# Kernel optimization log

Hardware: AMD Instinct MI355X
Metric: run time of the kernel (lower is better)

## Reference

```python
import jax, jax.numpy as jnp
import numpy as np

H = 1024          # hidden_size
K = 128           # MAX_LINK_CANDIDATES (cap applies to both keys and values)
EPS = 1e-8


def _spatial_features(kb, vb):
    """kb: [B,K,4] key boxes, vb: [B,V,4] value boxes -> [B,K,V,8].
    Vectorized version of _compute_spatial_features_pair over all (key,value) pairs."""
    kcx = (kb[..., 0] + kb[..., 2]) / 2
    kcy = (kb[..., 1] + kb[..., 3]) / 2
    vcx = (vb[..., 0] + vb[..., 2]) / 2
    vcy = (vb[..., 1] + vb[..., 3]) / 2
    dx = vcx[:, None, :] - kcx[:, :, None]                      # [B,K,V]
    dy = vcy[:, None, :] - kcy[:, :, None]
    dist = jnp.sqrt(dx ** 2 + dy ** 2 + EPS)
    angle = jnp.arctan2(dy, dx)
    kh = kb[..., 3] - kb[..., 1]
    vh = vb[..., 3] - vb[..., 1]
    h_ov = jnp.clip(jnp.minimum(kb[..., 3][:, :, None], vb[..., 3][:, None, :])
                    - jnp.maximum(kb[..., 1][:, :, None], vb[..., 1][:, None, :]), 0)
    h_align = h_ov / (jnp.minimum(kh[:, :, None], vh[:, None, :]) + EPS)
    kw = kb[..., 2] - kb[..., 0]
    vw = vb[..., 2] - vb[..., 0]
    v_ov = jnp.clip(jnp.minimum(kb[..., 2][:, :, None], vb[..., 2][:, None, :])
                    - jnp.maximum(kb[..., 0][:, :, None], vb[..., 0][:, None, :]), 0)
    v_align = v_ov / (jnp.minimum(kw[:, :, None], vw[:, None, :]) + EPS)
    area_ratio = (vh * vw)[:, None, :] / ((kh * kw)[:, :, None] + EPS)
    aspect = (vw / (vh + EPS))[:, None, :] / ((kw / (kh + EPS))[:, :, None])
    return jnp.stack([dx, dy, dist, angle, h_align, v_align, area_ratio, aspect], axis=-1)


def setup_inputs() -> dict:
    key = jax.random.key(0)
    ks = jax.random.split(key, 20)
    B, S = 4, 2048
    sequence_output = jax.random.normal(ks[0], (B, S, H), dtype=jnp.float32)
    entity_logits = jax.random.normal(ks[1], (B, S, 3), dtype=jnp.float32)
    base = jax.random.uniform(ks[2], (B, S, 2), dtype=jnp.float32) * 0.9
    size = jax.random.uniform(ks[3], (B, S, 2), dtype=jnp.float32) * 0.09 + 0.01
    bboxes = jnp.concatenate([base, base + size], axis=-1)      # valid x1<x2, y1<y2
    attention_mask = jnp.ones((B, S), dtype=jnp.int32)
    s = 1.0 / np.sqrt(H)
    inp = {
        "sequence_output": sequence_output,
        "entity_logits": entity_logits,
        "bboxes": bboxes,
        "attention_mask": attention_mask,
        "Wk": jax.random.normal(ks[4], (H, H), jnp.float32) * s,
        "bk": jnp.zeros((H,), jnp.float32),
        "Wv": jax.random.normal(ks[5], (H, H), jnp.float32) * s,
        "bv": jnp.zeros((H,), jnp.float32),
        "Wbil": jax.random.normal(ks[6], (H, H), jnp.float32) * s,   # bilinear weight (out=1 squeezed)
        "bbil": jnp.zeros((), jnp.float32),
        "Ws1": jax.random.normal(ks[7], (8, 64), jnp.float32) * (1.0 / np.sqrt(8)),
        "bs1": jnp.zeros((64,), jnp.float32),
        "Ws2": jax.random.normal(ks[8], (64, 32), jnp.float32) * (1.0 / np.sqrt(64)),
        "bs2": jnp.zeros((32,), jnp.float32),
        "Wf1": jax.random.normal(ks[9], (33, 16), jnp.float32) * (1.0 / np.sqrt(33)),
        "bf1": jnp.zeros((16,), jnp.float32),
        "Wf2": jax.random.normal(ks[10], (16, 1), jnp.float32) * 0.25,
        "bf2": jnp.zeros((1,), jnp.float32),
    }
    return inp


def reference(sequence_output, entity_logits, bboxes, attention_mask,
              Wk, bk, Wv, bv, Wbil, bbil, Ws1, bs1, Ws2, bs2, Wf1, bf1, Wf2, bf2):
    # Candidate selection: top-K tokens by class confidence among predicted keys/values.
    probs = jax.nn.softmax(entity_logits, axis=-1)
    preds = jnp.argmax(entity_logits, axis=-1)                  # [B,S]
    valid = attention_mask == 1
    key_conf = jnp.where((preds == 1) & valid, probs[..., 1], -jnp.inf)
    val_conf = jnp.where((preds == 2) & valid, probs[..., 2], -jnp.inf)
    _, key_idx = jax.lax.top_k(key_conf, K)                     # [B,K]
    _, val_idx = jax.lax.top_k(val_conf, K)

    seq_k = jnp.take_along_axis(sequence_output, key_idx[..., None], axis=1)  # [B,K,H]
    seq_v = jnp.take_along_axis(sequence_output, val_idx[..., None], axis=1)
    key_reps = seq_k @ Wk + bk                                  # dropout is identity at eval
    val_reps = seq_v @ Wv + bv

    # Bilinear scoring: k^T W v  -> [B,K,V] (chunking in torch is a memory detail, same math)
    biaffine = jnp.einsum('bkh,hg,bvg->bkv', key_reps, Wbil, val_reps) + bbil

    key_boxes = jnp.take_along_axis(bboxes, key_idx[..., None], axis=1)       # [B,K,4]
    val_boxes = jnp.take_along_axis(bboxes, val_idx[..., None], axis=1)
    sf = _spatial_features(key_boxes, val_boxes)                              # [B,K,V,8]
    spatial = jax.nn.relu(sf @ Ws1 + bs1) @ Ws2 + bs2                         # [B,K,V,32]

    combined = jnp.concatenate([biaffine[..., None], spatial], axis=-1)       # [B,K,V,33]
    scores = (jax.nn.relu(combined @ Wf1 + bf1) @ Wf2 + bf2)[..., 0]          # [B,K,V]
    return scores, key_idx, val_idx
```

## Files before the change

kernel.cpp:

```cpp
#include <hip/hip_runtime.h>
#include <hip/hip_bf16.h>
#include <math.h>

#define B_ 4
#define S_ 2048
#define H_ 1024
#define KC 128
#define EPSF 1e-8f

typedef __attribute__((ext_vector_type(8))) short bf16x8;
typedef __attribute__((ext_vector_type(4))) float f32x4;

#define B2F_LO(u) __uint_as_float((u) << 16)
#define B2F_HI(u) __uint_as_float((u) & 0xffff0000u)

static __device__ inline unsigned short f2b(float f) {
    unsigned u = __float_as_uint(f);
    return (unsigned short)((u + 0x7fffu + ((u >> 16) & 1u)) >> 16);
}

static __device__ inline void gload16(const void* g, void* l) {
    __builtin_amdgcn_global_load_lds(
        (const __attribute__((address_space(1))) unsigned int*)g,
        (__attribute__((address_space(3))) unsigned int*)l, 16, 0, 0);
}

static __device__ inline unsigned long long shflx64(unsigned long long v, int m) {
    int lo = __shfl_xor((int)(unsigned)(v & 0xffffffffull), m, 64);
    int hi = __shfl_xor((int)(unsigned)(v >> 32), m, 64);
    return ((unsigned long long)(unsigned)hi << 32) | (unsigned)lo;
}

#define CROSS_STAGE(k, j) do {                                              \
    const int lm = (j) >> 3;                                                \
    const bool upL  = (((lane) * 8) & (k)) == 0;                            \
    const bool lowr = ((lane) & lm) == 0;                                   \
    _Pragma("unroll")                                                       \
    for (int r = 0; r < 8; ++r) {                                           \
        unsigned long long o = shflx64(e[r], lm);                           \
        e[r] = ((upL == lowr) == (e[r] < o)) ? e[r] : o;                    \
    }                                                                       \
} while (0)

#define INTRA_STAGE(j, k) do {                                              \
    _Pragma("unroll")                                                       \
    for (int r = 0; r < 8; ++r) if (!(r & (j))) {                           \
        bool up = ((((lane) * 8 + r) & (k)) == 0);                          \
        unsigned long long a = e[r], b = e[r | (j)];                        \
        if (up ? (a > b) : (a < b)) { e[r] = b; e[r | (j)] = a; }           \
    }                                                                       \
} while (0)

static __device__ inline void wave_sort512(unsigned long long e[8], int lane) {
    INTRA_STAGE(1, 2);
    INTRA_STAGE(2, 4);  INTRA_STAGE(1, 4);
    INTRA_STAGE(4, 8);  INTRA_STAGE(2, 8);  INTRA_STAGE(1, 8);
    CROSS_STAGE(16, 8);
    INTRA_STAGE(4, 16); INTRA_STAGE(2, 16); INTRA_STAGE(1, 16);
    CROSS_STAGE(32, 16); CROSS_STAGE(32, 8);
    INTRA_STAGE(4, 32); INTRA_STAGE(2, 32); INTRA_STAGE(1, 32);
    CROSS_STAGE(64, 32); CROSS_STAGE(64, 16); CROSS_STAGE(64, 8);
    INTRA_STAGE(4, 64); INTRA_STAGE(2, 64); INTRA_STAGE(1, 64);
    CROSS_STAGE(128, 64); CROSS_STAGE(128, 32); CROSS_STAGE(128, 16);
    CROSS_STAGE(128, 8);
    INTRA_STAGE(4, 128); INTRA_STAGE(2, 128); INTRA_STAGE(1, 128);
    CROSS_STAGE(256, 128); CROSS_STAGE(256, 64); CROSS_STAGE(256, 32);
    CROSS_STAGE(256, 16); CROSS_STAGE(256, 8);
    INTRA_STAGE(4, 256); INTRA_STAGE(2, 256); INTRA_STAGE(1, 256);
    CROSS_STAGE(512, 256); CROSS_STAGE(512, 128); CROSS_STAGE(512, 64);
    CROSS_STAGE(512, 32); CROSS_STAGE(512, 16); CROSS_STAGE(512, 8);
    INTRA_STAGE(4, 512); INTRA_STAGE(2, 512); INTRA_STAGE(1, 512);
}

static __device__ inline void topk_block(
    const float* logits, const int* mask, int blk,
    int* key_idx, int* val_idx, float* out_idx_base,
    unsigned long long* cand, int tid)
{
    const int b   = blk >> 1;
    const int cls = (blk & 1) ? 2 : 1;
    const int wv = tid >> 6, lane = tid & 63;
    unsigned long long e[8];
    #pragma unroll
    for (int r = 0; r < 8; ++r) {
        int s = wv * 512 + lane * 8 + r;
        float l0 = logits[(b * S_ + s) * 3 + 0];
        float l1 = logits[(b * S_ + s) * 3 + 1];
        float l2 = logits[(b * S_ + s) * 3 + 2];
        int pred = 0; float bl = l0;
        if (l1 > bl) { bl = l1; pred = 1; }
        if (l2 > bl) { bl = l2; pred = 2; }
        float c = -1.0f;
        if (pred == cls && mask[b * S_ + s] == 1) {
            double m = (double)bl;
            double e0 = exp((double)l0 - m);
            double e1 = exp((double)l1 - m);
            double e2 = exp((double)l2 - m);
            c = (float)(((cls == 1) ? e1 : e2) / (e0 + e1 + e2));
        }
        unsigned int u = __float_as_uint(c);
        unsigned int mono = (u & 0x80000000u) ? ~u : (u | 0x80000000u);
        e[r] = ((unsigned long long)(~mono) << 32) | (unsigned int)s;
    }
    wave_sort512(e, lane);
    if (lane < 16) {
        #pragma unroll
        for (int r = 0; r < 8; ++r) cand[wv * 128 + lane * 8 + r] = e[r];
    }
    __syncthreads();
    if (wv == 0) {
        #pragma unroll
        for (int r = 0; r < 8; ++r) e[r] = cand[lane * 8 + r];
        wave_sort512(e, lane);
        if (lane < 16) {
            int* idx_out = (blk & 1) ? (val_idx + b * KC) : (key_idx + b * KC);
            float* oidx  = out_idx_base + ((blk & 1) ? B_ * KC : 0) + b * KC;
            #pragma unroll
            for (int r = 0; r < 8; ++r) {
                int sel = (int)(e[r] & 0xffffffffu);
                idx_out[lane * 8 + r] = sel;
                oidx[lane * 8 + r] = (float)sel;
            }
        }
    }
}

__global__ __launch_bounds__(256) void prep_kernel(
    const float* __restrict__ Wk, const float* __restrict__ Wv,
    const float* __restrict__ Wbil, unsigned short* __restrict__ Wt,
    const float* __restrict__ logits, const int* __restrict__ mask,
    int* __restrict__ key_idx, int* __restrict__ val_idx,
    const float* __restrict__ Ws1, const float* __restrict__ Ws2,
    const float* __restrict__ Wf1,
    unsigned short* __restrict__ Ws1T_b, unsigned short* __restrict__ Ws2_b,
    unsigned short* __restrict__ Wf1T_b, float* __restrict__ Wf1c0,
    float* __restrict__ out_idx)
{
    __shared__ float tile[32][33];
    __shared__ unsigned long long cand[512];
    const int tid = threadIdx.x;
    if (blockIdx.x < 3072) {
        const int z = blockIdx.x >> 10;
        const int remb = blockIdx.x & 1023;
        const float* Win = (z == 0) ? Wk : (z == 1) ? Wv : Wbil;
        unsigned short* out = Wt + (size_t)z * H_ * H_;
        const int n0 = (remb & 31) * 32, k0 = (remb >> 5) * 32;
        const int r = tid >> 3, c0 = (tid & 7) * 4;
        float4 v = *(const float4*)(Win + (size_t)(k0 + r) * H_ + n0 + c0);
        tile[r][c0 + 0] = v.x; tile[r][c0 + 1] = v.y;
        tile[r][c0 + 2] = v.z; tile[r][c0 + 3] = v.w;
        __syncthreads();
        short4 o;
        o.x = (short)f2b(tile[c0 + 0][r]);
        o.y = (short)f2b(tile[c0 + 1][r]);
        o.z = (short)f2b(tile[c0 + 2][r]);
        o.w = (short)f2b(tile[c0 + 3][r]);
        *(short4*)(out + (size_t)(n0 + r) * H_ + k0 + c0) = o;
        return;
    }
    if (blockIdx.x == 3080) {
        for (int i = tid; i < 512; i += 256) {
            int j = i >> 3, ii = i & 7;
            Ws1T_b[i] = f2b(Ws1[ii * 64 + j]);
        }
        for (int i = tid; i < 2048; i += 256) Ws2_b[i] = f2b(Ws2[i]);
        for (int i = tid; i < 512; i += 256) {
            int t = i >> 5, q = i & 31;
            Wf1T_b[i] = f2b(Wf1[(1 + q) * 16 + t]);
        }
        if (tid < 16) Wf1c0[tid] = Wf1[tid];
        return;
    }
    topk_block(logits, mask, blockIdx.x - 3072, key_idx, val_idx, out_idx,
               cand, tid);
}

__global__ __launch_bounds__(256) void gatherconv_kernel(
    const float* __restrict__ seq,
    const int* __restrict__ key_idx, const int* __restrict__ val_idx,
    unsigned short* __restrict__ Abf)
{
    const int row = blockIdx.x;
    const int tid = threadIdx.x;
    int b, srow;
    if (row < 512) { b = row >> 7; srow = key_idx[row]; }
    else           { b = (row - 512) >> 7; srow = val_idx[row - 512]; }
    const float* src = seq + ((size_t)b * S_ + srow) * H_ + tid * 4;
    float4 v = *(const float4*)src;
    short4 o;
    o.x = (short)f2b(v.x); o.y = (short)f2b(v.y);
    o.z = (short)f2b(v.z); o.w = (short)f2b(v.w);
    *(short4*)(Abf + (size_t)row * H_ + tid * 4) = o;
}

__global__ __launch_bounds__(256) void gemm_lds_kernel(
    const unsigned short* __restrict__ Ab,
    const unsigned short* __restrict__ Wt,
    const float* __restrict__ b0, const float* __restrict__ b1,
    unsigned short* __restrict__ Cout)
{
    __shared__ __align__(16) char As[64 * 512];
    __shared__ __align__(16) char Bs[64 * 512];

    const int NW8 = gridDim.x >> 3;
    int sw = ((int)blockIdx.x & 7) * NW8 + ((int)blockIdx.x >> 3);
    const int z  = sw >> 7;
    const int r2 = sw & 127;
    const int n0 = (r2 >> 3) * 64;
    const int m0 = (r2 & 7) * 64;

    Ab   += (size_t)z * 512 * H_;
    Cout += (size_t)z * 512 * H_;
    const unsigned short* Wz = Wt + (size_t)z * H_ * H_;
    const float* bias = z ? b1 : b0;

    const int tid  = threadIdx.x;
    const int lane = tid & 63, wv = tid >> 6;
    const int r = lane & 15, g = lane >> 4;
    const int mh = (wv >> 1) * 32, nh = (wv & 1) * 32;

    f32x4 acc[2][2] = {};

    for (int k0 = 0; k0 < H_; k0 += 256) {
        #pragma unroll
        for (int q = 0; q < 8; ++q) {
            const int seg = wv * 8 + q;
            const int row = (seg << 1) | (lane >> 5);
            const int gch = (lane & 31) ^ (row & 7);
            gload16(Ab + (size_t)(m0 + row) * H_ + k0 + gch * 8,
                    As + seg * 1024);
            gload16(Wz + (size_t)(n0 + row) * H_ + k0 + gch * 8,
                    Bs + seg * 1024);
        }
        __syncthreads();
        #pragma unroll
        for (int kk = 0; kk < 8; ++kk) {
            const int c = kk * 4 + g;
            bf16x8 av[2], bv[2];
            #pragma unroll
            for (int i = 0; i < 2; ++i) {
                const int row = mh + i * 16 + r;
                av[i] = *(const bf16x8*)(As + row * 512 + ((c ^ (row & 7)) << 4));
            }
            #pragma unroll
            for (int j = 0; j < 2; ++j) {
                const int row = nh + j * 16 + r;
                bv[j] = *(const bf16x8*)(Bs + row * 512 + ((c ^ (row & 7)) << 4));
            }
            #pragma unroll
            for (int i = 0; i < 2; ++i)
                #pragma unroll
                for (int j = 0; j < 2; ++j)
                    acc[i][j] = __builtin_amdgcn_mfma_f32_16x16x32_bf16(
                        av[i], bv[j], acc[i][j], 0, 0, 0);
        }
        __syncthreads();
    }

    const int orow = (lane >> 4) * 4, ocol = lane & 15;
    #pragma unroll
    for (int i = 0; i < 2; ++i)
        #pragma unroll
        for (int j = 0; j < 2; ++j) {
            const int n = n0 + nh + j * 16 + ocol;
            const float bv_ = bias ? bias[n] : 0.0f;
            #pragma unroll
            for (int gg = 0; gg < 4; ++gg)
                Cout[(size_t)(m0 + mh + i * 16 + orow + gg) * H_ + n]
                    = f2b(acc[i][j][gg] + bv_);
        }
}

__global__ __launch_bounds__(512) void biasp_kernel(
    const unsigned short* __restrict__ kbt,
    const unsigned short* __restrict__ vrep,
    const float* __restrict__ bbil, const float* __restrict__ bboxes,
    const int* __restrict__ key_idx, const int* __restrict__ val_idx,
    const unsigned short* __restrict__ Ws1T_b,
    const float* __restrict__ bs1,
    const unsigned short* __restrict__ Ws2_b,
    const float* __restrict__ bs2,
    const unsigned short* __restrict__ Wf1T_b,
    const float* __restrict__ Wf1c0,
    const float* __restrict__ bf1,
    const float* __restrict__ Wf2, const float* __restrict__ bf2,
    float* __restrict__ out)
{
    __shared__ float part[8][16][16];
    __shared__ uint4 sW1[64];
    __shared__ uint4 sW2[256];
    __shared__ uint4 sWf[64];
    __shared__ float sbs1[64];
    __shared__ float sbs2[32];
    __shared__ float sWf1c0[16];
    __shared__ float sbf1[16];
    __shared__ float sWf2[16];

    const int tid = threadIdx.x;
    if (tid < 64)  sW1[tid] = ((const uint4*)Ws1T_b)[tid];
    if (tid < 256) sW2[tid] = ((const uint4*)Ws2_b)[tid];
    if (tid >= 256 && tid < 320) sWf[tid - 256] = ((const uint4*)Wf1T_b)[tid - 256];
    if (tid >= 320 && tid < 384) sbs1[tid - 320] = bs1[tid - 320];
    if (tid >= 384 && tid < 416) sbs2[tid - 384] = bs2[tid - 384];
    if (tid >= 416 && tid < 432) sWf1c0[tid - 416] = Wf1c0[tid - 416];
    if (tid >= 432 && tid < 448) sbf1[tid - 432] = bf1[tid - 432];
    if (tid >= 448 && tid < 464) sWf2[tid - 448] = Wf2[tid - 448];

    const int b = blockIdx.x >> 6;
    const int t = blockIdx.x & 63;
    const int m0 = (t >> 3) * 16, n0 = (t & 7) * 16;
    const int lane = tid & 63, wv = tid >> 6;
    const int r = lane & 15, kq = (lane >> 4) * 8;

    f32x4 acc = {};
    const unsigned short* a0 = kbt  + (size_t)(b * KC + m0 + r) * H_ + kq;
    const unsigned short* w0 = vrep + (size_t)(b * KC + n0 + r) * H_ + kq;
    #pragma unroll
    for (int kk = 0; kk < 4; ++kk) {
        int k0 = wv * 128 + kk * 32;
        acc = __builtin_amdgcn_mfma_f32_16x16x32_bf16(
            *(const bf16x8*)(a0 + k0), *(const bf16x8*)(w0 + k0), acc, 0, 0, 0);
    }
    const int orow = (lane >> 4) * 4, ocol = lane & 15;
    #pragma unroll
    for (int g = 0; g < 4; ++g) part[wv][orow + g][ocol] = acc[g];
    __syncthreads();

    if (tid >= 256) return;

    const int kl = tid >> 4, vl = tid & 15;
    float c0 = bbil[0];
    #pragma unroll
    for (int w = 0; w < 8; ++w) c0 += part[w][kl][vl];
    const int kg = m0 + kl, vg = n0 + vl;

    const float* kbx = bboxes + ((size_t)b * S_ + key_idx[b * KC + kg]) * 4;
    const float* vbx = bboxes + ((size_t)b * S_ + val_idx[b * KC + vg]) * 4;
    float k0_ = kbx[0], k1_ = kbx[1], k2_ = kbx[2], k3_ = kbx[3];
    float v0_ = vbx[0], v1_ = vbx[1], v2_ = vbx[2], v3_ = vbx[3];

    float kcx = (k0_ + k2_) * 0.5f, kcy = (k1_ + k3_) * 0.5f;
    float vcx = (v0_ + v2_) * 0.5f, vcy = (v1_ + v3_) * 0.5f;
    float dx = vcx - kcx, dy = vcy - kcy;
    float dist = sqrtf(dx * dx + dy * dy + EPSF);
    float angle = atan2f(dy, dx);
    float kh = k3_ - k1_, vh = v3_ - v1_, kw = k2_ - k0_, vw = v2_ - v0_;
    float h_ov = fmaxf(fminf(k3_, v3_) - fmaxf(k1_, v1_), 0.0f);
    float h_align = h_ov / (fminf(kh, vh) + EPSF);
    float v_ov = fmaxf(fminf(k2_, v2_) - fmaxf(k0_, v0_), 0.0f);
    float v_align = v_ov / (fminf(kw, vw) + EPSF);
    float area_ratio = (vh * vw) / (kh * kw + EPSF);
    float aspect = (vw / (vh + EPSF)) / (kw / (kh + EPSF));

    float4 sfa = {dx, dy, dist, angle};
    float4 sfb = {h_align, v_align, area_ratio, aspect};

    float h2[32];
    #pragma unroll
    for (int q = 0; q < 32; ++q) h2[q] = sbs2[q];

    #pragma unroll 4
    for (int j = 0; j < 64; ++j) {
        uint4 w1 = sW1[j];
        float a = sbs1[j]
                + sfa.x * B2F_LO(w1.x) + sfa.y * B2F_HI(w1.x)
                + sfa.z * B2F_LO(w1.y) + sfa.w * B2F_HI(w1.y)
                + sfb.x * B2F_LO(w1.z) + sfb.y * B2F_HI(w1.z)
                + sfb.z * B2F_LO(w1.w) + sfb.w * B2F_HI(w1.w);
        a = fmaxf(a, 0.0f);
        const uint4* w2 = &sW2[j * 4];
        #pragma unroll
        for (int q = 0; q < 4; ++q) {
            uint4 w = w2[q];
            h2[q*8+0] += a * B2F_LO(w.x); h2[q*8+1] += a * B2F_HI(w.x);
            h2[q*8+2] += a * B2F_LO(w.y); h2[q*8+3] += a * B2F_HI(w.y);
            h2[q*8+4] += a * B2F_LO(w.z); h2[q*8+5] += a * B2F_HI(w.z);
            h2[q*8+6] += a * B2F_LO(w.w); h2[q*8+7] += a * B2F_HI(w.w);
        }
    }
    float score = bf2[0];
    #pragma unroll
    for (int tt = 0; tt < 16; ++tt) {
        float f = sbf1[tt] + c0 * sWf1c0[tt];
        const uint4* w = &sWf[tt * 4];
        #pragma unroll
        for (int q = 0; q < 4; ++q) {
            uint4 ww = w[q];
            f += h2[q*8+0] * B2F_LO(ww.x) + h2[q*8+1] * B2F_HI(ww.x)
               + h2[q*8+2] * B2F_LO(ww.y) + h2[q*8+3] * B2F_HI(ww.y)
               + h2[q*8+4] * B2F_LO(ww.z) + h2[q*8+5] * B2F_HI(ww.z)
               + h2[q*8+6] * B2F_LO(ww.w) + h2[q*8+7] * B2F_HI(ww.w);
        }
        score += fmaxf(f, 0.0f) * sWf2[tt];
    }
    out[((size_t)b * KC + kg) * KC + vg] = score;
}

extern "C" void kernel_launch(void* const* d_in, const int* in_sizes, int n_in,
                              void* d_out, int out_size, void* d_ws, size_t ws_size,
                              hipStream_t stream) {
    const float* seq    = (const float*)d_in[0];
    const float* logits = (const float*)d_in[1];
    const float* bboxes = (const float*)d_in[2];
    const int*   mask   = (const int*)d_in[3];
    const float* Wk   = (const float*)d_in[4];
    const float* bk   = (const float*)d_in[5];
    const float* Wv   = (const float*)d_in[6];
    const float* bv   = (const float*)d_in[7];
    const float* Wbil = (const float*)d_in[8];
    const float* bbil = (const float*)d_in[9];
    const float* Ws1  = (const float*)d_in[10];
    const float* bs1  = (const float*)d_in[11];
    const float* Ws2  = (const float*)d_in[12];
    const float* bs2  = (const float*)d_in[13];
    const float* Wf1  = (const float*)d_in[14];
    const float* bf1  = (const float*)d_in[15];
    const float* Wf2  = (const float*)d_in[16];
    const float* bf2  = (const float*)d_in[17];

    float* out = (float*)d_out;
    char* ws = (char*)d_ws;

    int* key_idx = (int*)(ws + 64);
    int* val_idx = key_idx + B_ * KC;
    unsigned short* Wt   = (unsigned short*)(ws + 8192);
    unsigned short* Abf  = Wt + (size_t)3 * H_ * H_;
    unsigned short* reps = Abf + (size_t)1024 * H_;
    unsigned short* kbt  = reps + (size_t)1024 * H_;
    unsigned short* Ws1T_b = kbt + (size_t)512 * H_;
    unsigned short* Ws2_b  = Ws1T_b + 512;
    unsigned short* Wf1T_b = Ws2_b + 2048;
    float* Wf1c0 = (float*)(Wf1T_b + 512);

    prep_kernel<<<3081, 256, 0, stream>>>(Wk, Wv, Wbil, Wt,
                                          logits, mask, key_idx, val_idx,
                                          Ws1, Ws2, Wf1,
                                          Ws1T_b, Ws2_b, Wf1T_b, Wf1c0,
                                          out + B_ * KC * KC);
    gatherconv_kernel<<<1024, 256, 0, stream>>>(seq, key_idx, val_idx, Abf);
    gemm_lds_kernel<<<256, 256, 0, stream>>>(Abf, Wt, bk, bv, reps);
    gemm_lds_kernel<<<128, 256, 0, stream>>>(
        reps, Wt + (size_t)2 * H_ * H_, nullptr, nullptr, kbt);
    biasp_kernel<<<256, 512, 0, stream>>>(kbt, reps + (size_t)512 * H_,
                                          bbil, bboxes, key_idx, val_idx,
                                          Ws1T_b, bs1, Ws2_b, bs2,
                                          Wf1T_b, Wf1c0, bf1, Wf2, bf2, out);
}
```

Before: 72.53 us.

## Split fused biaffine+spatial MLP kernel into separate biaffine and MLP kernels

```diff
diff --git a/kernel.cpp b/kernel.cpp
--- a/kernel.cpp
+++ b/kernel.cpp
@@ -271,10 +271,44 @@
         }
 }
 
-__global__ __launch_bounds__(512) void biasp_kernel(
+__global__ __launch_bounds__(512) void biaffine_kernel(
     const unsigned short* __restrict__ kbt,
     const unsigned short* __restrict__ vrep,
-    const float* __restrict__ bbil, const float* __restrict__ bboxes,
+    const float* __restrict__ bbil,
+    float* __restrict__ out)
+{
+    __shared__ float part[8][16][16];
+    const int tid = threadIdx.x;
+    const int b = blockIdx.x >> 6;
+    const int t = blockIdx.x & 63;
+    const int m0 = (t >> 3) * 16, n0 = (t & 7) * 16;
+    const int lane = tid & 63, wv = tid >> 6;
+    const int r = lane & 15, kq = (lane >> 4) * 8;
+
+    f32x4 acc = {};
+    const unsigned short* a0 = kbt  + (size_t)(b * KC + m0 + r) * H_ + kq;
+    const unsigned short* w0 = vrep + (size_t)(b * KC + n0 + r) * H_ + kq;
+    #pragma unroll
+    for (int kk = 0; kk < 4; ++kk) {
+        int k0 = wv * 128 + kk * 32;
+        acc = __builtin_amdgcn_mfma_f32_16x16x32_bf16(
+            *(const bf16x8*)(a0 + k0), *(const bf16x8*)(w0 + k0), acc, 0, 0, 0);
+    }
+    const int orow = (lane >> 4) * 4, ocol = lane & 15;
+    #pragma unroll
+    for (int g = 0; g < 4; ++g) part[wv][orow + g][ocol] = acc[g];
+    __syncthreads();
+
+    if (tid >= 256) return;
+    const int kl = tid >> 4, vl = tid & 15;
+    float c0 = bbil[0];
+    #pragma unroll
+    for (int w = 0; w < 8; ++w) c0 += part[w][kl][vl];
+    out[((size_t)b * KC + m0 + kl) * KC + n0 + vl] = c0;
+}
+
+__global__ __launch_bounds__(128) void mlp_kernel(
+    const float* __restrict__ bboxes,
     const int* __restrict__ key_idx, const int* __restrict__ val_idx,
     const unsigned short* __restrict__ Ws1T_b,
     const float* __restrict__ bs1,
@@ -286,7 +320,6 @@
     const float* __restrict__ Wf2, const float* __restrict__ bf2,
     float* __restrict__ out)
 {
-    __shared__ float part[8][16][16];
     __shared__ uint4 sW1[64];
     __shared__ uint4 sW2[256];
     __shared__ uint4 sWf[64];
@@ -298,44 +331,23 @@
 
     const int tid = threadIdx.x;
     if (tid < 64)  sW1[tid] = ((const uint4*)Ws1T_b)[tid];
-    if (tid < 256) sW2[tid] = ((const uint4*)Ws2_b)[tid];
-    if (tid >= 256 && tid < 320) sWf[tid - 256] = ((const uint4*)Wf1T_b)[tid - 256];
-    if (tid >= 320 && tid < 384) sbs1[tid - 320] = bs1[tid - 320];
-    if (tid >= 384 && tid < 416) sbs2[tid - 384] = bs2[tid - 384];
-    if (tid >= 416 && tid < 432) sWf1c0[tid - 416] = Wf1c0[tid - 416];
-    if (tid >= 432 && tid < 448) sbf1[tid - 432] = bf1[tid - 432];
-    if (tid >= 448 && tid < 464) sWf2[tid - 448] = Wf2[tid - 448];
-
-    const int b = blockIdx.x >> 6;
-    const int t = blockIdx.x & 63;
-    const int m0 = (t >> 3) * 16, n0 = (t & 7) * 16;
-    const int lane = tid & 63, wv = tid >> 6;
-    const int r = lane & 15, kq = (lane >> 4) * 8;
-
-    f32x4 acc = {};
-    const unsigned short* a0 = kbt  + (size_t)(b * KC + m0 + r) * H_ + kq;
-    const unsigned short* w0 = vrep + (size_t)(b * KC + n0 + r) * H_ + kq;
-    #pragma unroll
-    for (int kk = 0; kk < 4; ++kk) {
-        int k0 = wv * 128 + kk * 32;
-        acc = __builtin_amdgcn_mfma_f32_16x16x32_bf16(
-            *(const bf16x8*)(a0 + k0), *(const bf16x8*)(w0 + k0), acc, 0, 0, 0);
-    }
-    const int orow = (lane >> 4) * 4, ocol = lane & 15;
-    #pragma unroll
-    for (int g = 0; g < 4; ++g) part[wv][orow + g][ocol] = acc[g];
+    for (int i = tid; i < 256; i += 128) sW2[i] = ((const uint4*)Ws2_b)[i];
+    if (tid < 64)  sWf[tid] = ((const uint4*)Wf1T_b)[tid];
+    if (tid >= 64 && tid < 128) sbs1[tid - 64] = bs1[tid - 64];
+    if (tid < 32)  sbs2[tid] = bs2[tid];
+    if (tid >= 32 && tid < 48)  sWf1c0[tid - 32] = Wf1c0[tid - 32];
+    if (tid >= 48 && tid < 64)  sbf1[tid - 48] = bf1[tid - 48];
+    if (tid >= 96 && tid < 112) sWf2[tid - 96] = Wf2[tid - 96];
     __syncthreads();
 
-    if (tid >= 256) return;
-
-    const int kl = tid >> 4, vl = tid & 15;
-    float c0 = bbil[0];
-    #pragma unroll
-    for (int w = 0; w < 8; ++w) c0 += part[w][kl][vl];
-    const int kg = m0 + kl, vg = n0 + vl;
-
-    const float* kbx = bboxes + ((size_t)b * S_ + key_idx[b * KC + kg]) * 4;
-    const float* vbx = bboxes + ((size_t)b * S_ + val_idx[b * KC + vg]) * 4;
+    const int gid = blockIdx.x * 128 + tid;
+    const int b = gid >> 14;
+    const int rem = gid & 16383;
+    const int k = rem >> 7;
+    const int v = rem & 127;
+
+    const float* kbx = bboxes + ((size_t)b * S_ + key_idx[b * KC + k]) * 4;
+    const float* vbx = bboxes + ((size_t)b * S_ + val_idx[b * KC + v]) * 4;
     float k0_ = kbx[0], k1_ = kbx[1], k2_ = kbx[2], k3_ = kbx[3];
     float v0_ = vbx[0], v1_ = vbx[1], v2_ = vbx[2], v3_ = vbx[3];
 
@@ -378,6 +390,7 @@
             h2[q*8+6] += a * B2F_LO(w.w); h2[q*8+7] += a * B2F_HI(w.w);
         }
     }
+    float c0 = out[gid];
     float score = bf2[0];
     #pragma unroll
     for (int tt = 0; tt < 16; ++tt) {
@@ -393,7 +406,7 @@
         }
         score += fmaxf(f, 0.0f) * sWf2[tt];
     }
-    out[((size_t)b * KC + kg) * KC + vg] = score;
+    out[gid] = score;
 }
 
 extern "C" void kernel_launch(void* const* d_in, const int* in_sizes, int n_in,
@@ -441,8 +454,9 @@
     gemm_lds_kernel<<<256, 256, 0, stream>>>(Abf, Wt, bk, bv, reps);
     gemm_lds_kernel<<<128, 256, 0, stream>>>(
         reps, Wt + (size_t)2 * H_ * H_, nullptr, nullptr, kbt);
-    biasp_kernel<<<256, 512, 0, stream>>>(kbt, reps + (size_t)512 * H_,
-                                          bbil, bboxes, key_idx, val_idx,
-                                          Ws1T_b, bs1, Ws2_b, bs2,
-                                          Wf1T_b, Wf1c0, bf1, Wf2, bf2, out);
-}
+    biaffine_kernel<<<256, 512, 0, stream>>>(kbt, reps + (size_t)512 * H_,
+                                             bbil, out);
+    mlp_kernel<<<512, 128, 0, stream>>>(bboxes, key_idx, val_idx,
+                                        Ws1T_b, bs1, Ws2_b, bs2,
+                                        Wf1T_b, Wf1c0, bf1, Wf2, bf2, out);
+}
```

New measurement: 83.04 us. 14.5% more time.
